# Optimization experiments

Measured on AMD Instinct MI355X. Metric: run time of the kernel, lower is better.

Reference implementation:

```python
import jax, jax.numpy as jnp
import numpy as np

LAMBDA_COORD = 5.0
LAMBDA_NOOBJ = 0.5
CELL_SILE = 1.0 / 7.0


def setup_inputs() -> dict:
    key = jax.random.key(0)
    k1, k2, k3 = jax.random.split(key, 3)
    B, S, C = 16384, 49, 30
    predictions = jax.random.normal(k1, (B, S, C), dtype=jnp.float32)
    targets = jax.random.uniform(k2, (B, S, C), dtype=jnp.float32)
    # confidence column must be exactly 0/1 for the equality masks in the loss
    obj = (jax.random.uniform(k3, (B, S)) < 0.3).astype(jnp.float32)
    targets = targets.at[:, :, 4].set(obj)
    return {"predictions": predictions, "targets": targets}


def reference(predictions, targets):
    # Flatten cells: row-major order matches torch boolean indexing order.
    p = predictions.reshape(-1, 30)  # [N, 30], N = B*49
    t = targets.reshape(-1, 30)
    conf = t[:, 4]
    coord_mask = conf == 1.0
    noobj = (conf == 0.0).astype(p.dtype)

    # no-object confidence loss on columns [4, 9]
    noobj_loss = LAMBDA_NOOBJ * jnp.sum(
        noobj * ((p[:, 4] - t[:, 4]) ** 2 + (p[:, 9] - t[:, 9]) ** 2))

    # The original zips N_obj rows against N_obj//2 output rows, so only the
    # first floor(N_obj/2) object cells (in flattened order) contribute.
    n_obj = jnp.sum(coord_mask.astype(jnp.int32))
    rank = jnp.cumsum(coord_mask.astype(jnp.int32))  # 1-indexed object rank
    w = (coord_mask & (rank <= n_obj // 2)).astype(p.dtype)

    # pred boxes: columns [0:4] and [5:9] -> [N, 2, 4]
    pb = p[:, :10].reshape(-1, 2, 5)[..., :4]
    # faithful in-place transform: a = xy*c - wh ; b = a*c + wh
    pa = pb[..., :2] * CELL_SILE - pb[..., 2:4]
    pbb = pa * CELL_SILE + pb[..., 2:4]
    pbox = jnp.concatenate([pa, pbb], axis=-1)  # [N, 2, 4]

    tb = jnp.square(t[:, :4])
    ta = tb[:, :2] * CELL_SILE - tb[:, 2:4]
    tbb = ta * CELL_SILE + tb[:, 2:4]
    tbox = jnp.concatenate([ta, tbb], axis=-1)  # [N, 4]

    # torchvision.ops.box_iou, batched over cells
    lt = jnp.maximum(pbox[..., :2], tbox[:, None, :2])
    rb = jnp.minimum(pbox[..., 2:], tbox[:, None, 2:])
    whd = jnp.clip(rb - lt, 0.0)
    inter = whd[..., 0] * whd[..., 1]  # [N, 2]
    area_p = (pbox[..., 2] - pbox[..., 0]) * (pbox[..., 3] - pbox[..., 1])
    area_t = (tbox[:, 2] - tbox[:, 0]) * (tbox[:, 3] - tbox[:, 1])
    iou = inter / (area_p + area_t[:, None] - inter)  # [N, 2]

    idx = jnp.argmax(iou, axis=1)  # responsible box per cell
    sel = jnp.take_along_axis(p[:, :10].reshape(-1, 2, 5),
                              idx[:, None, None], axis=1)[:, 0, :]  # [N, 5]
    obj_idx = jnp.argmax(t[:, 10:], axis=1)
    sel_cls = jnp.take_along_axis(p[:, 10:], obj_idx[:, None], axis=1)[:, 0]

    center = jnp.sum(w * jnp.sum((sel[:, :2] - t[:, :2]) ** 2, axis=1))
    xywh = jnp.sum(w * jnp.sum((sel[:, 2:4] - t[:, 2:4]) ** 2, axis=1))
    # original compares column 5 twice (confidence_loss and classier_loss are
    # the same term): pred class prob vs constant 1
    conf_l = jnp.sum(w * (sel_cls - 1.0) ** 2)
    cls_l = jnp.sum(w * (sel_cls - 1.0) ** 2)

    return LAMBDA_COORD * (center + xywh + conf_l + cls_l) + noobj_loss
```

## Files before the change

kernel.cpp:

```cpp
#include <hip/hip_runtime.h>


#define ROWS 256
#define COLS 30
#define NB   3136
#define RC   (ROWS * COLS)
#define RC4  (RC / 4)

__device__ __forceinline__ void row_compute(const float* __restrict__ P,
                                            const float* __restrict__ T,
                                            bool& coord, float& r, float& noo) {
    const float C = 1.0f / 7.0f;
    float conf = T[4];
    coord = (conf == 1.0f);
    noo = 0.0f;
    if (conf == 0.0f) {
        float d4 = P[4] - conf;
        float d9 = P[9] - T[9];
        noo = d4 * d4 + d9 * d9;
    }
    float t0 = T[0], t1 = T[1], t2 = T[2], t3 = T[3];
    float tb0 = t0 * t0, tb1 = t1 * t1, tb2 = t2 * t2, tb3 = t3 * t3;
    float tax = tb0 * C - tb2, tay = tb1 * C - tb3;
    float tbx = tax * C + tb2, tby = tay * C + tb3;
    float areaT = (tbx - tax) * (tby - tay);
    float iou0 = 0.0f, iou1 = 0.0f;
#pragma unroll
    for (int b = 0; b < 2; ++b) {
        float px = P[5 * b + 0], py = P[5 * b + 1];
        float pw = P[5 * b + 2], ph = P[5 * b + 3];
        float pax = px * C - pw, pay = py * C - ph;
        float pbx = pax * C + pw, pby = pay * C + ph;
        float ltx = fmaxf(pax, tax), lty = fmaxf(pay, tay);
        float rbx = fminf(pbx, tbx), rby = fminf(pby, tby);
        float wx = fmaxf(rbx - ltx, 0.0f), wy = fmaxf(rby - lty, 0.0f);
        float inter = wx * wy;
        float areaP = (pbx - pax) * (pby - pay);
        float iou = inter / (areaP + areaT - inter);
        if (b == 0) iou0 = iou; else iou1 = iou;
    }
    int idx = (iou1 > iou0) ? 1 : 0;
    int so = 5 * idx;
    float sx = P[so + 0], sy = P[so + 1], sw = P[so + 2], sh = P[so + 3];
    float best = T[10]; int bi = 0;
#pragma unroll
    for (int j = 1; j < 20; ++j) {
        float v = T[10 + j];
        if (v > best) { best = v; bi = j; }
    }
    float pc = P[10 + bi];
    float d0 = sx - t0, d1 = sy - t1, d2 = sw - t2, d3 = sh - t3;
    float dc = pc - 1.0f;
    r = d0 * d0 + d1 * d1 + d2 * d2 + d3 * d3 + 2.0f * dc * dc;
}

__device__ __forceinline__ void stage_block(const float* __restrict__ p,
                                            const float* __restrict__ t,
                                            float* lp, float* lt,
                                            int blockId, int tid) {
    const float4* p4 = (const float4*)(p + (size_t)blockId * RC);
    const float4* t4 = (const float4*)(t + (size_t)blockId * RC);
    float4* lp4 = (float4*)lp;
    float4* lt4 = (float4*)lt;
    float4 a[8], b[8];
#pragma unroll
    for (int it = 0; it < 7; ++it) a[it] = p4[tid + it * 256];
#pragma unroll
    for (int it = 0; it < 7; ++it) b[it] = t4[tid + it * 256];
    bool tail = (tid < (RC4 - 7 * 256));
    if (tail) { a[7] = p4[tid + 1792]; b[7] = t4[tid + 1792]; }
#pragma unroll
    for (int it = 0; it < 7; ++it) lp4[tid + it * 256] = a[it];
#pragma unroll
    for (int it = 0; it < 7; ++it) lt4[tid + it * 256] = b[it];
    if (tail) { lp4[tid + 1792] = a[7]; lt4[tid + 1792] = b[7]; }
    __syncthreads();
}

__global__ __launch_bounds__(256) void yolo_k1(const float* __restrict__ p,
                                               const float* __restrict__ t,
                                               int* __restrict__ cnt,
                                               float* __restrict__ sumR,
                                               float* __restrict__ noo) {
    __shared__ float lp[RC];
    __shared__ float lt[RC];
    __shared__ float wr[4], wn[4];
    __shared__ int wc[4];
    int tid = threadIdx.x;
    stage_block(p, t, lp, lt, blockIdx.x, tid);

    bool coord; float r, nt;
    row_compute(lp + tid * COLS, lt + tid * COLS, coord, r, nt);
    float rl = coord ? r : 0.0f;

    unsigned long long bal = __ballot(coord);
    int c = (int)__popcll(bal);
#pragma unroll
    for (int off = 32; off > 0; off >>= 1) {
        rl += __shfl_down(rl, off);
        nt += __shfl_down(nt, off);
    }
    int wave = tid >> 6, lane = tid & 63;
    if (lane == 0) { wr[wave] = rl; wn[wave] = nt; wc[wave] = c; }
    __syncthreads();
    if (tid == 0) {
        cnt[blockIdx.x]  = wc[0] + wc[1] + wc[2] + wc[3];
        sumR[blockIdx.x] = wr[0] + wr[1] + wr[2] + wr[3];
        noo[blockIdx.x]  = wn[0] + wn[1] + wn[2] + wn[3];
    }
}

__global__ __launch_bounds__(256) void yolo_k2(const int* __restrict__ cnt,
                                               const float* __restrict__ sumR,
                                               const float* __restrict__ noo,
                                               float* __restrict__ scal) {
    __shared__ int   s_i[256];
    __shared__ float s_f[256];
    __shared__ int   s_scan[256];
    __shared__ int   s_running;
    __shared__ int   sh_nhalf;
    __shared__ float sh_noo;
    __shared__ int   sh_bstar, sh_kstar;
    int tid = threadIdx.x;

    int c = 0; float nf = 0.0f;
    for (int i = tid; i < NB; i += 256) { c += cnt[i]; nf += noo[i]; }
    s_i[tid] = c; s_f[tid] = nf;
    __syncthreads();
    for (int s = 128; s > 0; s >>= 1) {
        if (tid < s) { s_i[tid] += s_i[tid + s]; s_f[tid] += s_f[tid + s]; }
        __syncthreads();
    }
    if (tid == 0) {
        sh_nhalf = s_i[0] >> 1;
        sh_noo = s_f[0];
        s_running = 0;
        sh_bstar = -1;
        sh_kstar = 0;
    }
    __syncthreads();
    int n_half = sh_nhalf;

    float fullAcc = 0.0f;
    for (int chunk = 0; chunk < NB; chunk += 256) {
        int i = chunk + tid;
        int ci = (i < NB) ? cnt[i] : 0;
        s_scan[tid] = ci;
        __syncthreads();
        for (int off = 1; off < 256; off <<= 1) {
            int add = (tid >= off) ? s_scan[tid - off] : 0;
            __syncthreads();
            s_scan[tid] += add;
            __syncthreads();
        }
        int incl = s_scan[tid];
        int prefix = s_running + incl - ci;
        if (i < NB && ci > 0) {
            if (prefix + ci <= n_half) {
                fullAcc += sumR[i];
            } else if (prefix < n_half) {
                sh_bstar = i;
                sh_kstar = n_half - prefix;
            }
        }
        __syncthreads();
        if (tid == 255) s_running += incl;
        __syncthreads();
    }

    s_f[tid] = fullAcc;
    __syncthreads();
    for (int s = 128; s > 0; s >>= 1) {
        if (tid < s) s_f[tid] += s_f[tid + s];
        __syncthreads();
    }
    if (tid == 0) {
        scal[0] = 5.0f * s_f[0] + 0.5f * sh_noo;
        ((int*)scal)[1] = sh_bstar;
        ((int*)scal)[2] = sh_kstar;
    }
}

__global__ __launch_bounds__(256) void yolo_k3(const float* __restrict__ p,
                                               const float* __restrict__ t,
                                               const float* __restrict__ scal,
                                               float* __restrict__ out) {
    __shared__ float lp[RC];
    __shared__ float lt[RC];
    __shared__ int   wcnt[4];
    __shared__ float pr[4];
    int tid = threadIdx.x;
    int bstar = ((const int*)scal)[1];
    int kstar = ((const int*)scal)[2];
    float base = scal[0];
    float total = 0.0f;
    if (bstar >= 0) {
        stage_block(p, t, lp, lt, bstar, tid);
        bool coord; float r, nt;
        row_compute(lp + tid * COLS, lt + tid * COLS, coord, r, nt);
        unsigned long long bal = __ballot(coord);
        int wave = tid >> 6, lane = tid & 63;
        if (lane == 0) wcnt[wave] = (int)__popcll(bal);
        __syncthreads();
        int waveoff = 0;
        for (int wi = 0; wi < wave; ++wi) waveoff += wcnt[wi];
        unsigned long long below_incl =
            (lane == 63) ? bal : (bal & ((1ull << (lane + 1)) - 1ull));
        int rank = waveoff + (int)__popcll(below_incl);
        float val = (coord && rank <= kstar) ? r : 0.0f;
#pragma unroll
        for (int off = 32; off > 0; off >>= 1) val += __shfl_down(val, off);
        if (lane == 0) pr[wave] = val;
        __syncthreads();
        if (tid == 0) total = pr[0] + pr[1] + pr[2] + pr[3];
    }
    if (tid == 0) out[0] = base + 5.0f * total;
}

extern "C" void kernel_launch(void* const* d_in, const int* in_sizes, int n_in,
                              void* d_out, int out_size, void* d_ws, size_t ws_size,
                              hipStream_t stream) {
    (void)in_sizes; (void)n_in; (void)out_size; (void)ws_size;
    const float* p = (const float*)d_in[0];
    const float* t = (const float*)d_in[1];
    char* ws = (char*)d_ws;
    int*   cnt  = (int*)ws;
    float* sumR = (float*)(ws + (size_t)NB * 4);
    float* noo  = (float*)(ws + (size_t)NB * 8);
    float* scal = (float*)(ws + (size_t)NB * 12);
    float* out  = (float*)d_out;

    yolo_k1<<<NB, 256, 0, stream>>>(p, t, cnt, sumR, noo);
    yolo_k2<<<1, 256, 0, stream>>>(cnt, sumR, noo, scal);
    yolo_k3<<<1, 256, 0, stream>>>(p, t, scal, out);
}
```

Measured before the change: 247.8 us.

## Load rows directly into registers and merge scan and tail kernels

```diff
diff --git a/kernel.cpp b/kernel.cpp
--- a/kernel.cpp
+++ b/kernel.cpp
@@ -1,11 +1,8 @@
 #include <hip/hip_runtime.h>
 
 
-#define ROWS 256
 #define COLS 30
 #define NB   3136
-#define RC   (ROWS * COLS)
-#define RC4  (RC / 4)
 
 __device__ __forceinline__ void row_compute(const float* __restrict__ P,
                                             const float* __restrict__ T,
@@ -40,41 +37,29 @@
         if (b == 0) iou0 = iou; else iou1 = iou;
     }
     int idx = (iou1 > iou0) ? 1 : 0;
-    int so = 5 * idx;
-    float sx = P[so + 0], sy = P[so + 1], sw = P[so + 2], sh = P[so + 3];
-    float best = T[10]; int bi = 0;
+    float sx = idx ? P[5] : P[0];
+    float sy = idx ? P[6] : P[1];
+    float sw = idx ? P[7] : P[2];
+    float sh = idx ? P[8] : P[3];
+    float best = T[10]; float pc = P[10];
 #pragma unroll
     for (int j = 1; j < 20; ++j) {
         float v = T[10 + j];
-        if (v > best) { best = v; bi = j; }
-    }
-    float pc = P[10 + bi];
+        if (v > best) { best = v; pc = P[10 + j]; }
+    }
     float d0 = sx - t0, d1 = sy - t1, d2 = sw - t2, d3 = sh - t3;
     float dc = pc - 1.0f;
     r = d0 * d0 + d1 * d1 + d2 * d2 + d3 * d3 + 2.0f * dc * dc;
 }
 
-__device__ __forceinline__ void stage_block(const float* __restrict__ p,
-                                            const float* __restrict__ t,
-                                            float* lp, float* lt,
-                                            int blockId, int tid) {
-    const float4* p4 = (const float4*)(p + (size_t)blockId * RC);
-    const float4* t4 = (const float4*)(t + (size_t)blockId * RC);
-    float4* lp4 = (float4*)lp;
-    float4* lt4 = (float4*)lt;
-    float4 a[8], b[8];
-#pragma unroll
-    for (int it = 0; it < 7; ++it) a[it] = p4[tid + it * 256];
-#pragma unroll
-    for (int it = 0; it < 7; ++it) b[it] = t4[tid + it * 256];
-    bool tail = (tid < (RC4 - 7 * 256));
-    if (tail) { a[7] = p4[tid + 1792]; b[7] = t4[tid + 1792]; }
-#pragma unroll
-    for (int it = 0; it < 7; ++it) lp4[tid + it * 256] = a[it];
-#pragma unroll
-    for (int it = 0; it < 7; ++it) lt4[tid + it * 256] = b[it];
-    if (tail) { lp4[tid + 1792] = a[7]; lt4[tid + 1792] = b[7]; }
-    __syncthreads();
+__device__ __forceinline__ void load_row(const float* __restrict__ src,
+                                         long row, float* dst) {
+    const float2* s2 = (const float2*)(src + row * (long)COLS);
+#pragma unroll
+    for (int i = 0; i < 15; ++i) {
+        float2 v = s2[i];
+        dst[2 * i] = v.x; dst[2 * i + 1] = v.y;
+    }
 }
 
 __global__ __launch_bounds__(256) void yolo_k1(const float* __restrict__ p,
@@ -82,15 +67,16 @@
                                                int* __restrict__ cnt,
                                                float* __restrict__ sumR,
                                                float* __restrict__ noo) {
-    __shared__ float lp[RC];
-    __shared__ float lt[RC];
     __shared__ float wr[4], wn[4];
     __shared__ int wc[4];
     int tid = threadIdx.x;
-    stage_block(p, t, lp, lt, blockIdx.x, tid);
+    long row = (long)blockIdx.x * 256 + tid;
+    float Pr[30], Tr[30];
+    load_row(p, row, Pr);
+    load_row(t, row, Tr);
 
     bool coord; float r, nt;
-    row_compute(lp + tid * COLS, lt + tid * COLS, coord, r, nt);
+    row_compute(Pr, Tr, coord, r, nt);
     float rl = coord ? r : 0.0f;
 
     unsigned long long bal = __ballot(coord);
@@ -113,108 +99,93 @@
 __global__ __launch_bounds__(256) void yolo_k2(const int* __restrict__ cnt,
                                                const float* __restrict__ sumR,
                                                const float* __restrict__ noo,
-                                               float* __restrict__ scal) {
-    __shared__ int   s_i[256];
-    __shared__ float s_f[256];
-    __shared__ int   s_scan[256];
-    __shared__ int   s_running;
-    __shared__ int   sh_nhalf;
-    __shared__ float sh_noo;
-    __shared__ int   sh_bstar, sh_kstar;
+                                               const float* __restrict__ p,
+                                               const float* __restrict__ t,
+                                               float* __restrict__ out) {
+    __shared__ int   wsum[4];
+    __shared__ float wf[4], wn2[4];
+    __shared__ int   s_bstar, s_kstar;
+    __shared__ float s_base;
+    __shared__ int   s_wcnt[4];
     int tid = threadIdx.x;
-
-    int c = 0; float nf = 0.0f;
-    for (int i = tid; i < NB; i += 256) { c += cnt[i]; nf += noo[i]; }
-    s_i[tid] = c; s_f[tid] = nf;
-    __syncthreads();
-    for (int s = 128; s > 0; s >>= 1) {
-        if (tid < s) { s_i[tid] += s_i[tid + s]; s_f[tid] += s_f[tid + s]; }
-        __syncthreads();
-    }
-    if (tid == 0) {
-        sh_nhalf = s_i[0] >> 1;
-        sh_noo = s_f[0];
-        s_running = 0;
-        sh_bstar = -1;
-        sh_kstar = 0;
-    }
-    __syncthreads();
-    int n_half = sh_nhalf;
-
-    float fullAcc = 0.0f;
-    for (int chunk = 0; chunk < NB; chunk += 256) {
-        int i = chunk + tid;
-        int ci = (i < NB) ? cnt[i] : 0;
-        s_scan[tid] = ci;
-        __syncthreads();
-        for (int off = 1; off < 256; off <<= 1) {
-            int add = (tid >= off) ? s_scan[tid - off] : 0;
-            __syncthreads();
-            s_scan[tid] += add;
-            __syncthreads();
-        }
-        int incl = s_scan[tid];
-        int prefix = s_running + incl - ci;
-        if (i < NB && ci > 0) {
-            if (prefix + ci <= n_half) {
-                fullAcc += sumR[i];
-            } else if (prefix < n_half) {
-                sh_bstar = i;
-                sh_kstar = n_half - prefix;
+    int lane = tid & 63, wave = tid >> 6;
+    if (tid == 0) { s_bstar = -1; s_kstar = 0; }
+
+    const int PER = 13;
+    int start = tid * PER;
+    int end = min(NB, start + PER);
+
+    int cloc = 0; float nloc = 0.0f;
+    for (int i = start; i < end; ++i) { cloc += cnt[i]; nloc += noo[i]; }
+
+    int incl = cloc;
+#pragma unroll
+    for (int off = 1; off < 64; off <<= 1) {
+        int v = __shfl_up(incl, off);
+        if (lane >= off) incl += v;
+    }
+    if (lane == 63) wsum[wave] = incl;
+    __syncthreads();
+    int woff = 0;
+#pragma unroll
+    for (int w = 0; w < 4; ++w) woff += (w < wave) ? wsum[w] : 0;
+    int ex = woff + incl - cloc;
+    int n_obj = wsum[0] + wsum[1] + wsum[2] + wsum[3];
+    int n_half = n_obj >> 1;
+
+    float acc = 0.0f;
+    int running = ex;
+    for (int i = start; i < end; ++i) {
+        int ci = cnt[i];
+        if (ci > 0) {
+            if (running + ci <= n_half) {
+                acc += sumR[i];
+            } else if (running < n_half) {
+                s_bstar = i;
+                s_kstar = n_half - running;
             }
         }
-        __syncthreads();
-        if (tid == 255) s_running += incl;
-        __syncthreads();
-    }
-
-    s_f[tid] = fullAcc;
-    __syncthreads();
-    for (int s = 128; s > 0; s >>= 1) {
-        if (tid < s) s_f[tid] += s_f[tid + s];
-        __syncthreads();
-    }
-    if (tid == 0) {
-        scal[0] = 5.0f * s_f[0] + 0.5f * sh_noo;
-        ((int*)scal)[1] = sh_bstar;
-        ((int*)scal)[2] = sh_kstar;
-    }
-}
-
-__global__ __launch_bounds__(256) void yolo_k3(const float* __restrict__ p,
-                                               const float* __restrict__ t,
-                                               const float* __restrict__ scal,
-                                               float* __restrict__ out) {
-    __shared__ float lp[RC];
-    __shared__ float lt[RC];
-    __shared__ int   wcnt[4];
-    __shared__ float pr[4];
-    int tid = threadIdx.x;
-    int bstar = ((const int*)scal)[1];
-    int kstar = ((const int*)scal)[2];
-    float base = scal[0];
+        running += ci;
+    }
+
+#pragma unroll
+    for (int off = 32; off > 0; off >>= 1) {
+        acc  += __shfl_down(acc, off);
+        nloc += __shfl_down(nloc, off);
+    }
+    if (lane == 0) { wf[wave] = acc; wn2[wave] = nloc; }
+    __syncthreads();
+    if (tid == 0)
+        s_base = 5.0f * (wf[0] + wf[1] + wf[2] + wf[3])
+               + 0.5f * (wn2[0] + wn2[1] + wn2[2] + wn2[3]);
+    __syncthreads();
+
+    int bstar = s_bstar, kstar = s_kstar;
     float total = 0.0f;
     if (bstar >= 0) {
-        stage_block(p, t, lp, lt, bstar, tid);
+        long row = (long)bstar * 256 + tid;
+        float Pr[30], Tr[30];
+        load_row(p, row, Pr);
+        load_row(t, row, Tr);
         bool coord; float r, nt;
-        row_compute(lp + tid * COLS, lt + tid * COLS, coord, r, nt);
+        row_compute(Pr, Tr, coord, r, nt);
         unsigned long long bal = __ballot(coord);
-        int wave = tid >> 6, lane = tid & 63;
-        if (lane == 0) wcnt[wave] = (int)__popcll(bal);
+        if (lane == 0) s_wcnt[wave] = (int)__popcll(bal);
         __syncthreads();
         int waveoff = 0;
-        for (int wi = 0; wi < wave; ++wi) waveoff += wcnt[wi];
+#pragma unroll
+        for (int w = 0; w < 4; ++w) waveoff += (w < wave) ? s_wcnt[w] : 0;
         unsigned long long below_incl =
             (lane == 63) ? bal : (bal & ((1ull << (lane + 1)) - 1ull));
         int rank = waveoff + (int)__popcll(below_incl);
         float val = (coord && rank <= kstar) ? r : 0.0f;
 #pragma unroll
         for (int off = 32; off > 0; off >>= 1) val += __shfl_down(val, off);
-        if (lane == 0) pr[wave] = val;
+        if (lane == 0) wf[wave] = val;
         __syncthreads();
-        if (tid == 0) total = pr[0] + pr[1] + pr[2] + pr[3];
-    }
-    if (tid == 0) out[0] = base + 5.0f * total;
+        if (tid == 0) total = wf[0] + wf[1] + wf[2] + wf[3];
+    }
+    if (tid == 0) out[0] = s_base + 5.0f * total;
 }
 
 extern "C" void kernel_launch(void* const* d_in, const int* in_sizes, int n_in,
@@ -227,10 +198,8 @@
     int*   cnt  = (int*)ws;
     float* sumR = (float*)(ws + (size_t)NB * 4);
     float* noo  = (float*)(ws + (size_t)NB * 8);
-    float* scal = (float*)(ws + (size_t)NB * 12);
     float* out  = (float*)d_out;
 
     yolo_k1<<<NB, 256, 0, stream>>>(p, t, cnt, sumR, noo);
-    yolo_k2<<<1, 256, 0, stream>>>(cnt, sumR, noo, scal);
-    yolo_k3<<<1, 256, 0, stream>>>(p, t, scal, out);
-}
+    yolo_k2<<<1, 256, 0, stream>>>(cnt, sumR, noo, p, t, out);
+}
```

Result: faster. 232.2 us (-6.3%).
